# Optimization experiments

Measured on AMD Instinct MI355X. Metric: run time of the kernel, lower is better.

## Reference

```python
import jax, jax.numpy as jnp
import numpy as np

N = 100000
IN_PLANES = 64
OUT_PLANES = 64
SHARE = 8
NSAMPLE = 16


def setup_inputs() -> dict:
    key = jax.random.key(0)
    ks = jax.random.split(key, 20)
    f32 = jnp.float32
    s = lambda fan_in: 1.0 / np.sqrt(fan_in)
    inp = {}
    inp['p'] = jax.random.normal(ks[0], (N, 3), f32)
    inp['x'] = jax.random.normal(ks[1], (N, IN_PLANES), f32)
    inp['knn_idx'] = jax.random.randint(ks[2], (N, NSAMPLE), 0, N, jnp.int64)
    # channelMixMLPs01: Linear(3+in, nsample) -> ReLU -> Bilinear(ns, ns, ns)
    inp['W01'] = jax.random.uniform(ks[3], (3 + IN_PLANES, NSAMPLE), f32, -s(3 + IN_PLANES), s(3 + IN_PLANES))
    inp['b01'] = jnp.zeros((NSAMPLE,), f32)
    inp['Wbil'] = jax.random.uniform(ks[4], (NSAMPLE, NSAMPLE, NSAMPLE), f32, -s(NSAMPLE), s(NSAMPLE))
    inp['bbil'] = jnp.zeros((NSAMPLE,), f32)
    # linear_p: Linear(3,3) -> BN(3) -> ReLU -> Linear(3, out)
    inp['Wp1'] = jax.random.uniform(ks[5], (3, 3), f32, -s(3), s(3))
    inp['bp1'] = jnp.zeros((3,), f32)
    inp['bnp_s'] = jnp.ones((3,), f32)   # BN folded (inference): scale = gamma/sqrt(var+eps)
    inp['bnp_b'] = jnp.zeros((3,), f32)  # shift = beta - mean*scale
    inp['Wp2'] = jax.random.uniform(ks[6], (3, OUT_PLANES), f32, -s(3), s(3))
    inp['bp2'] = jnp.zeros((OUT_PLANES,), f32)
    # channelMixMLPs02
    mid = OUT_PLANES
    inp['W2a'] = jax.random.uniform(ks[7], (2 * NSAMPLE, mid), f32, -s(2 * NSAMPLE), s(2 * NSAMPLE))
    inp['bn2a_s'] = jnp.ones((mid,), f32)
    inp['bn2a_b'] = jnp.zeros((mid,), f32)
    inp['W2b'] = jax.random.uniform(ks[8], (mid, mid // SHARE), f32, -s(mid), s(mid))
    inp['bn2b_s'] = jnp.ones((mid // SHARE,), f32)
    inp['bn2b_b'] = jnp.zeros((mid // SHARE,), f32)
    inp['W2c'] = jax.random.uniform(ks[9], (mid // SHARE, OUT_PLANES // SHARE), f32, -s(mid // SHARE), s(mid // SHARE))
    inp['b2c'] = jnp.zeros((OUT_PLANES // SHARE,), f32)
    # channelMixMLPs03: Linear(in, out)
    inp['W3'] = jax.random.uniform(ks[10], (IN_PLANES, OUT_PLANES), f32, -s(IN_PLANES), s(IN_PLANES))
    inp['b3'] = jnp.zeros((OUT_PLANES,), f32)
    return inp


def reference(p, x, knn_idx, W01, b01, Wbil, bbil, Wp1, bp1, bnp_s, bnp_b,
              Wp2, bp2, W2a, bn2a_s, bn2a_b, W2b, bn2b_s, bn2b_b, W2c, b2c,
              W3, b3):
    n, k = knn_idx.shape
    out_planes = W3.shape[1]
    share = SHARE
    # queryandgroup(use_xyz=True): gather neighbors, relative xyz concat features
    p_r = p[knn_idx] - p[:, None, :]                      # [n,k,3]
    x_knn_in = jnp.concatenate([p_r, x[knn_idx]], -1)     # [n,k,3+in]
    xf = x_knn_in.reshape(n * k, -1)
    # channelMixMLPs01: Linear -> ReLU -> Bilinear(e, e)
    e = jax.nn.relu(xf @ W01 + b01)                       # [nk, ns]
    e = jnp.einsum('ni,oij,nj->no', e, Wbil, e) + bbil    # [nk, ns]
    # linear_p on relative coords
    pe = p_r.reshape(-1, 3) @ Wp1 + bp1
    pe = jax.nn.relu(pe * bnp_s + bnp_b)
    pe = pe @ Wp2 + bp2                                   # [nk, out]
    p_embed = pe.reshape(n, k, out_planes)
    # shrink_p: (n k (a b)) -> sum over a -> (nk, b=nsample)
    a = out_planes // k
    shrink = pe.reshape(n * k, a, k).sum(1)               # [nk, ns]
    ef = jnp.concatenate([e, shrink], -1)                 # [nk, 2*ns]
    # channelMixMLPs02
    h = jax.nn.relu((ef @ W2a) * bn2a_s + bn2a_b)
    h = jax.nn.relu((h @ W2b) * bn2b_s + bn2b_b)
    h = h @ W2c + b2c                                     # [nk, out/share]
    w = jax.nn.softmax(h.reshape(n, k, -1), axis=1)       # softmax over neighbors
    # channelMixMLPs03 then gather
    x_v = (x @ W3 + b3)[knn_idx]                          # [n,k,out]
    x_knn = (x_v + p_embed).reshape(n, k, share, out_planes // share)
    x_knn = (x_knn * w[:, :, None, :]).reshape(n, k, out_planes)
    x_out = x_knn.sum(1)                                  # [n,out]
    return (x_out, x_knn, knn_idx, p_r)
```

## Files before the change

### kernel.cpp

```cpp
#include <hip/hip_runtime.h>

#define NPTS 100000
#define NK   1600000

typedef __attribute__((ext_vector_type(8))) short bf16x8;
typedef __attribute__((ext_vector_type(4))) float f32x4;
typedef union { bf16x8 v; unsigned u[4]; } fragu;

#define MFMA(a,b,c) __builtin_amdgcn_mfma_f32_16x16x32_bf16((a),(b),(c),0,0,0)

#define WS_W01  0
#define WS_WBIL 1536
#define WS_W2A  5632
#define WS_W2B  7680
#define WS_WPE  8704
#define WS_BYTES 21504

__device__ inline unsigned cvtpk(float lo, float hi) {
  unsigned r;
  asm("v_cvt_pk_bf16_f32 %0, %1, %2" : "=v"(r) : "v"(lo), "v"(hi));
  return r;
}
__device__ inline short bfr(float f) {
  unsigned u = __float_as_uint(f);
  u += 0x7fff + ((u >> 16) & 1);
  return (short)(u >> 16);
}
__device__ inline float bflo(unsigned u) { return __uint_as_float(u << 16); }
__device__ inline float bfhi(unsigned u) { return __uint_as_float(u & 0xffff0000u); }

__global__ __launch_bounds__(256) void k_prep(
    const float* __restrict__ W01, const float* __restrict__ b01,
    const float* __restrict__ Wbil,
    const float* __restrict__ W2a, const float* __restrict__ W2b,
    const float* __restrict__ Wp2, const float* __restrict__ bp2,
    short* __restrict__ ws)
{
  const int t = threadIdx.x;
  for (int i = t; i < 3 * 512; i += 256) {
    int tt = i & 7, l = (i >> 3) & 63, kc = i >> 9;
    int o = l & 15, k = kc * 32 + ((l >> 4) << 3) + tt;
    float v = 0.f;
    if (k < 64) v = W01[(3 + k) * 16 + o];
    else if (k < 67) v = W01[(k - 64) * 16 + o];
    else if (k == 67) v = b01[o];
    ws[WS_W01 + i] = bfr(v);
  }
  for (int i = t; i < 8 * 512; i += 256) {
    int tt = i & 7, l = (i >> 3) & 63, kc = i >> 9;
    int o = l & 15, k = kc * 32 + ((l >> 4) << 3) + tt;
    ws[WS_WBIL + i] = bfr(Wbil[o * 256 + k]);
  }
  for (int i = t; i < 4 * 512; i += 256) {
    int tt = i & 7, l = (i >> 3) & 63, nt = i >> 9;
    int c = nt * 16 + (l & 15), k = ((l >> 4) << 3) + tt;
    ws[WS_W2A + i] = bfr(W2a[k * 64 + c]);
  }
  for (int i = t; i < 2 * 512; i += 256) {
    int tt = i & 7, l = (i >> 3) & 63, kc = i >> 9;
    int m = l & 15, k = kc * 32 + ((l >> 4) << 3) + tt;
    ws[WS_W2B + i] = bfr(m < 8 ? W2b[k * 8 + m] : 0.f);
  }
  for (int i = t; i < 4 * 512; i += 256) {
    int tt = i & 7, l = (i >> 3) & 63, nt = i >> 9;
    int c = nt * 16 + (l & 15), k = ((l >> 4) << 3) + tt;
    float v = 0.f;
    if (k < 3) v = Wp2[k * 64 + c]; else if (k == 3) v = bp2[c];
    ws[WS_WPE + i] = bfr(v);
  }
}

__global__ __launch_bounds__(256) void k_xw3(
    const float* __restrict__ x, const float* __restrict__ W3,
    const float* __restrict__ b3, float* __restrict__ y)
{
  int t = blockIdx.x * 256 + threadIdx.x;
  int i = __builtin_amdgcn_readfirstlane(t >> 6);
  int c = t & 63;
  if (i >= NPTS) return;
  const float* xr = x + i * 64;
  float acc = b3[c];
#pragma unroll
  for (int k = 0; k < 64; ++k)
    acc = fmaf(xr[k], W3[k * 64 + c], acc);
  y[i * 64 + c] = acc;
}

__global__ __launch_bounds__(256, 5) void k_main(
    const float* __restrict__ p, const float* __restrict__ x,
    const int* __restrict__ knn, const short* __restrict__ wsf,
    const float* __restrict__ Wp1, const float* __restrict__ bp1,
    const float* __restrict__ bnp_s, const float* __restrict__ bnp_b,
    const float* __restrict__ bbil,
    const float* __restrict__ bn2a_s, const float* __restrict__ bn2a_b,
    const float* __restrict__ bn2b_s, const float* __restrict__ bn2b_b,
    const float* __restrict__ W2c, const float* __restrict__ b2c,
    const float* __restrict__ Wp2, const float* __restrict__ bp2,
    const float* __restrict__ y,
    float* __restrict__ x_out, float* __restrict__ x_knn,
    float* __restrict__ knn_f, float* __restrict__ p_r)
{
  const int tid  = threadIdx.x;
  const int lane = tid & 63;
  const int mloc = lane & 15;
  const int kblk = lane >> 4;
  const int row  = blockIdx.x * 256 + tid;
  const int n    = row >> 4;
  const int j    = row & 15;
  const int idx  = knn[row];

  const float pr0 = p[idx * 3 + 0] - p[n * 3 + 0];
  const float pr1 = p[idx * 3 + 1] - p[n * 3 + 1];
  const float pr2 = p[idx * 3 + 2] - p[n * 3 + 2];

  float q0, q1, q2;
  {
    float v0 = bp1[0] + pr0 * Wp1[0] + pr1 * Wp1[3] + pr2 * Wp1[6];
    float v1 = bp1[1] + pr0 * Wp1[1] + pr1 * Wp1[4] + pr2 * Wp1[7];
    float v2 = bp1[2] + pr0 * Wp1[2] + pr1 * Wp1[5] + pr2 * Wp1[8];
    q0 = fmaxf(fmaf(v0, bnp_s[0], bnp_b[0]), 0.f);
    q1 = fmaxf(fmaf(v1, bnp_s[1], bnp_b[1]), 0.f);
    q2 = fmaxf(fmaf(v2, bnp_s[2], bnp_b[2]), 0.f);
  }

#define FR(off, idx_) (((const bf16x8*)wsf)[(off) / 8 + (idx_)])

  unsigned epk[4][2];
  {
    bf16x8 bw0 = FR(WS_W01, 0 * 64 + lane);
    bf16x8 bw1 = FR(WS_W01, 1 * 64 + lane);
    bf16x8 bw2 = FR(WS_W01, 2 * 64 + lane);
    const float4* x4 = (const float4*)x;
#pragma unroll
    for (int g = 0; g < 4; ++g) {
      const int src = g * 16 + mloc;
      int   ridx = __shfl(idx, src, 64);
      float p0s  = __shfl(pr0, src, 64);
      float p1s  = __shfl(pr1, src, 64);
      float p2s  = __shfl(pr2, src, 64);
      f32x4 acc = {0.f, 0.f, 0.f, 0.f};
      {
        float4 xa = x4[ridx * 16 + kblk * 2];
        float4 xb = x4[ridx * 16 + kblk * 2 + 1];
        fragu B;
        B.u[0] = cvtpk(xa.x, xa.y); B.u[1] = cvtpk(xa.z, xa.w);
        B.u[2] = cvtpk(xb.x, xb.y); B.u[3] = cvtpk(xb.z, xb.w);
        acc = MFMA(bw0, B.v, acc);
      }
      {
        float4 xa = x4[ridx * 16 + 8 + kblk * 2];
        float4 xb = x4[ridx * 16 + 9 + kblk * 2];
        fragu B;
        B.u[0] = cvtpk(xa.x, xa.y); B.u[1] = cvtpk(xa.z, xa.w);
        B.u[2] = cvtpk(xb.x, xb.y); B.u[3] = cvtpk(xb.z, xb.w);
        acc = MFMA(bw1, B.v, acc);
      }
      {
        fragu B;
        B.u[0] = (kblk == 0) ? cvtpk(p0s, p1s) : 0u;
        B.u[1] = (kblk == 0) ? cvtpk(p2s, 1.f) : 0u;
        B.u[2] = 0u; B.u[3] = 0u;
        acc = MFMA(bw2, B.v, acc);
      }
      epk[g][0] = cvtpk(fmaxf(acc[0], 0.f), fmaxf(acc[1], 0.f));
      epk[g][1] = cvtpk(fmaxf(acc[2], 0.f), fmaxf(acc[3], 0.f));
    }
  }

  unsigned h2p[4][2];
#pragma unroll
  for (int g = 0; g < 4; ++g) {
    float er[16];
    {
      unsigned a0 = __shfl(epk[g][0], mloc, 64);
      unsigned a1 = __shfl(epk[g][1], mloc, 64);
      unsigned b0 = __shfl(epk[g][0], mloc + 16, 64);
      unsigned b1 = __shfl(epk[g][1], mloc + 16, 64);
      unsigned c0 = __shfl(epk[g][0], mloc + 32, 64);
      unsigned c1 = __shfl(epk[g][1], mloc + 32, 64);
      unsigned d0 = __shfl(epk[g][0], mloc + 48, 64);
      unsigned d1 = __shfl(epk[g][1], mloc + 48, 64);
      er[0] = bflo(a0);  er[1] = bfhi(a0);  er[2]  = bflo(a1); er[3]  = bfhi(a1);
      er[4] = bflo(b0);  er[5] = bfhi(b0);  er[6]  = bflo(b1); er[7]  = bfhi(b1);
      er[8] = bflo(c0);  er[9] = bfhi(c0);  er[10] = bflo(c1); er[11] = bfhi(c1);
      er[12] = bflo(d0); er[13] = bfhi(d0); er[14] = bflo(d1); er[15] = bfhi(d1);
    }
    const int jhsel = kblk & 1, ihsel = kblk >> 1;
    float ej[8];
#pragma unroll
    for (int t = 0; t < 8; ++t) ej[t] = jhsel ? er[8 + t] : er[t];
    f32x4 acc2;
    {
      f32x4 bb = *(const f32x4*)&bbil[kblk * 4];
      acc2 = bb;
#pragma unroll
      for (int kc = 0; kc < 8; ++kc) {
        bf16x8 wb = FR(WS_WBIL, kc * 64 + lane);
        float ei = ihsel ? er[2 * kc + 1] : er[2 * kc];
        fragu B;
        B.u[0] = cvtpk(ei * ej[0], ei * ej[1]);
        B.u[1] = cvtpk(ei * ej[2], ei * ej[3]);
        B.u[2] = cvtpk(ei * ej[4], ei * ej[5]);
        B.u[3] = cvtpk(ei * ej[6], ei * ej[7]);
        acc2 = MFMA(wb, B.v, acc2);
      }
    }
    f32x4 shq;
    {
      const int src = g * 16 + mloc;
      float q0s = __shfl(q0, src, 64);
      float q1s = __shfl(q1, src, 64);
      float q2s = __shfl(q2, src, 64);
      fragu B;
      B.u[0] = (kblk == 0) ? cvtpk(q0s, q1s) : 0u;
      B.u[1] = (kblk == 0) ? cvtpk(q2s, 1.f) : 0u;
      B.u[2] = 0u; B.u[3] = 0u;
      f32x4 z = {0.f, 0.f, 0.f, 0.f};
      f32x4 s0 = MFMA(FR(WS_WPE, 0 * 64 + lane), B.v, z);
      f32x4 s1 = MFMA(FR(WS_WPE, 1 * 64 + lane), B.v, z);
      f32x4 s2 = MFMA(FR(WS_WPE, 2 * 64 + lane), B.v, z);
      f32x4 s3 = MFMA(FR(WS_WPE, 3 * 64 + lane), B.v, z);
#pragma unroll
      for (int r = 0; r < 4; ++r) shq[r] = s0[r] + s1[r] + s2[r] + s3[r];
    }
    unsigned pe2_0 = cvtpk(acc2[0], acc2[1]);
    unsigned pe2_1 = cvtpk(acc2[2], acc2[3]);
    unsigned psh_0 = cvtpk(shq[0], shq[1]);
    unsigned psh_1 = cvtpk(shq[2], shq[3]);
    fragu Bef;
    {
      const int s1l = mloc + 32 * (kblk & 1);
      const int s2l = s1l + 16;
      unsigned a0 = __shfl(pe2_0, s1l, 64);
      unsigned a1 = __shfl(pe2_1, s1l, 64);
      unsigned a2 = __shfl(pe2_0, s2l, 64);
      unsigned a3 = __shfl(pe2_1, s2l, 64);
      unsigned b0 = __shfl(psh_0, s1l, 64);
      unsigned b1 = __shfl(psh_1, s1l, 64);
      unsigned b2 = __shfl(psh_0, s2l, 64);
      unsigned b3 = __shfl(psh_1, s2l, 64);
      const bool lo2 = (kblk < 2);
      Bef.u[0] = lo2 ? a0 : b0; Bef.u[1] = lo2 ? a1 : b1;
      Bef.u[2] = lo2 ? a2 : b2; Bef.u[3] = lo2 ? a3 : b3;
    }
    unsigned pha[8];
#pragma unroll
    for (int nt = 0; nt < 4; ++nt) {
      bf16x8 wa = FR(WS_W2A, nt * 64 + lane);
      f32x4 z = {0.f, 0.f, 0.f, 0.f};
      f32x4 c = MFMA(wa, Bef.v, z);
      f32x4 sA = *(const f32x4*)&bn2a_s[nt * 16 + kblk * 4];
      f32x4 bA = *(const f32x4*)&bn2a_b[nt * 16 + kblk * 4];
      float h0 = fmaxf(fmaf(c[0], sA[0], bA[0]), 0.f);
      float h1 = fmaxf(fmaf(c[1], sA[1], bA[1]), 0.f);
      float h2 = fmaxf(fmaf(c[2], sA[2], bA[2]), 0.f);
      float h3 = fmaxf(fmaf(c[3], sA[3], bA[3]), 0.f);
      pha[nt * 2 + 0] = cvtpk(h0, h1);
      pha[nt * 2 + 1] = cvtpk(h2, h3);
    }
    {
      const int sAl = mloc + 32 * (kblk & 1);
      const int sBl = sAl + 16;
      const bool lo2 = (kblk < 2);
      fragu B0, B1;
      {
        unsigned a0 = __shfl(pha[0], sAl, 64), a1 = __shfl(pha[1], sAl, 64);
        unsigned a2 = __shfl(pha[0], sBl, 64), a3 = __shfl(pha[1], sBl, 64);
        unsigned b0 = __shfl(pha[2], sAl, 64), b1 = __shfl(pha[3], sAl, 64);
        unsigned b2 = __shfl(pha[2], sBl, 64), b3 = __shfl(pha[3], sBl, 64);
        B0.u[0] = lo2 ? a0 : b0; B0.u[1] = lo2 ? a1 : b1;
        B0.u[2] = lo2 ? a2 : b2; B0.u[3] = lo2 ? a3 : b3;
      }
      {
        unsigned a0 = __shfl(pha[4], sAl, 64), a1 = __shfl(pha[5], sAl, 64);
        unsigned a2 = __shfl(pha[4], sBl, 64), a3 = __shfl(pha[5], sBl, 64);
        unsigned b0 = __shfl(pha[6], sAl, 64), b1 = __shfl(pha[7], sAl, 64);
        unsigned b2 = __shfl(pha[6], sBl, 64), b3 = __shfl(pha[7], sBl, 64);
        B1.u[0] = lo2 ? a0 : b0; B1.u[1] = lo2 ? a1 : b1;
        B1.u[2] = lo2 ? a2 : b2; B1.u[3] = lo2 ? a3 : b3;
      }
      f32x4 acc3 = {0.f, 0.f, 0.f, 0.f};
      acc3 = MFMA(FR(WS_W2B, 0 * 64 + lane), B0.v, acc3);
      acc3 = MFMA(FR(WS_W2B, 1 * 64 + lane), B1.v, acc3);
      f32x4 s = *(const f32x4*)&bn2b_s[(kblk & 1) * 4];
      f32x4 b = *(const f32x4*)&bn2b_b[(kblk & 1) * 4];
      float v0 = fmaxf(fmaf(acc3[0], s[0], b[0]), 0.f);
      float v1 = fmaxf(fmaf(acc3[1], s[1], b[1]), 0.f);
      float v2 = fmaxf(fmaf(acc3[2], s[2], b[2]), 0.f);
      float v3 = fmaxf(fmaf(acc3[3], s[3], b[3]), 0.f);
      h2p[g][0] = cvtpk(v0, v1);
      h2p[g][1] = cvtpk(v2, v3);
    }
  }

  unsigned hp0 = 0, hp1 = 0, hp2 = 0, hp3 = 0;
#pragma unroll
  for (int g = 0; g < 4; ++g) {
    unsigned t0 = __shfl(h2p[g][0], mloc, 64);
    unsigned t1 = __shfl(h2p[g][1], mloc, 64);
    unsigned t2 = __shfl(h2p[g][0], mloc + 16, 64);
    unsigned t3 = __shfl(h2p[g][1], mloc + 16, 64);
    const bool mine = (kblk == g);
    hp0 = mine ? t0 : hp0; hp1 = mine ? t1 : hp1;
    hp2 = mine ? t2 : hp2; hp3 = mine ? t3 : hp3;
  }
  float h2r[8];
  h2r[0] = bflo(hp0); h2r[1] = bfhi(hp0); h2r[2] = bflo(hp1); h2r[3] = bfhi(hp1);
  h2r[4] = bflo(hp2); h2r[5] = bfhi(hp2); h2r[6] = bflo(hp3); h2r[7] = bfhi(hp3);

  float h3[8];
#pragma unroll
  for (int b = 0; b < 8; ++b) h3[b] = b2c[b];
#pragma unroll
  for (int m = 0; m < 8; ++m) {
    float r = h2r[m];
#pragma unroll
    for (int b = 0; b < 8; ++b) h3[b] = fmaf(r, W2c[m * 8 + b], h3[b]);
  }
  float wv[8];
#pragma unroll
  for (int b = 0; b < 8; ++b) {
    float mx = h3[b];
    mx = fmaxf(mx, __shfl_xor(mx, 1, 16));
    mx = fmaxf(mx, __shfl_xor(mx, 2, 16));
    mx = fmaxf(mx, __shfl_xor(mx, 4, 16));
    mx = fmaxf(mx, __shfl_xor(mx, 8, 16));
    float ex = __expf(h3[b] - mx);
    float s = ex;
    s += __shfl_xor(s, 1, 16);
    s += __shfl_xor(s, 2, 16);
    s += __shfl_xor(s, 4, 16);
    s += __shfl_xor(s, 8, 16);
    wv[b] = ex / s;
  }

  const float4* y4 = (const float4*)y;
  float* xkrow = x_knn + (long long)row * 64;
  float xo[4] = {0.f, 0.f, 0.f, 0.f};
#pragma unroll
  for (int h = 0; h < 2; ++h) {
    float4 yv[8];
#pragma unroll
    for (int u = 0; u < 8; ++u) yv[u] = y4[idx * 16 + h * 8 + u];
    f32x4 vout[8];
#pragma unroll
    for (int u = 0; u < 8; ++u) {
      float comp[4] = {yv[u].x, yv[u].y, yv[u].z, yv[u].w};
#pragma unroll
      for (int cc = 0; cc < 4; ++cc) {
        const int c = h * 32 + u * 4 + cc;
        float pe = bp2[c] + q0 * Wp2[c] + q1 * Wp2[64 + c] + q2 * Wp2[128 + c];
        float val = (comp[cc] + pe) * wv[c & 7];
        vout[u][cc] = val;
        float r = val;
        r += __shfl_xor(r, 1, 16);
        r += __shfl_xor(r, 2, 16);
        r += __shfl_xor(r, 4, 16);
        r += __shfl_xor(r, 8, 16);
        if (j == (c & 15)) xo[c >> 4] = r;
      }
    }
#pragma unroll
    for (int u = 0; u < 8; ++u)
      *(f32x4*)(xkrow + h * 32 + u * 4) = vout[u];
  }
#pragma unroll
  for (int g = 0; g < 4; ++g)
    x_out[n * 64 + g * 16 + j] = xo[g];

  if (knn_f) {
    knn_f[row] = (float)idx;
    p_r[row * 3 + 0] = pr0;
    p_r[row * 3 + 1] = pr1;
    p_r[row * 3 + 2] = pr2;
  }
}

__global__ __launch_bounds__(256) void k_tail(
    const float* __restrict__ p, const int* __restrict__ knn,
    float* __restrict__ knn_f, float* __restrict__ p_r)
{
  int row = blockIdx.x * 256 + threadIdx.x;
  if (row >= NK) return;
  int n = row >> 4;
  int idx = knn[row];
  knn_f[row] = (float)idx;
  p_r[row * 3 + 0] = p[idx * 3 + 0] - p[n * 3 + 0];
  p_r[row * 3 + 1] = p[idx * 3 + 1] - p[n * 3 + 1];
  p_r[row * 3 + 2] = p[idx * 3 + 2] - p[n * 3 + 2];
}

extern "C" void kernel_launch(void* const* d_in, const int* in_sizes, int n_in,
                              void* d_out, int out_size, void* d_ws, size_t ws_size,
                              hipStream_t stream)
{
  const float* p    = (const float*)d_in[0];
  const float* x    = (const float*)d_in[1];
  const int*   knn  = (const int*)d_in[2];
  const float* W01  = (const float*)d_in[3];
  const float* b01  = (const float*)d_in[4];
  const float* Wbil = (const float*)d_in[5];
  const float* bbil = (const float*)d_in[6];
  const float* Wp1  = (const float*)d_in[7];
  const float* bp1  = (const float*)d_in[8];
  const float* bnps = (const float*)d_in[9];
  const float* bnpb = (const float*)d_in[10];
  const float* Wp2  = (const float*)d_in[11];
  const float* bp2  = (const float*)d_in[12];
  const float* W2a  = (const float*)d_in[13];
  const float* s2a  = (const float*)d_in[14];
  const float* b2a  = (const float*)d_in[15];
  const float* W2b  = (const float*)d_in[16];
  const float* s2b  = (const float*)d_in[17];
  const float* b2b  = (const float*)d_in[18];
  const float* W2c  = (const float*)d_in[19];
  const float* b2c  = (const float*)d_in[20];
  const float* W3   = (const float*)d_in[21];
  const float* b3   = (const float*)d_in[22];

  float* outF  = (float*)d_out;
  float* x_out = outF;
  float* x_knn = outF + 6400000;
  float* knn_f = outF + 108800000;
  float* p_r   = outF + 110400000;
  short* wsf   = (short*)d_ws;

  const size_t yBytes = (size_t)NPTS * 64 * sizeof(float);
  const bool bigWs = ws_size >= (size_t)WS_BYTES + yBytes;
  float* y = bigWs ? (float*)((char*)d_ws + WS_BYTES) : knn_f;

  k_prep<<<1, 256, 0, stream>>>(W01, b01, Wbil, W2a, W2b, Wp2, bp2, wsf);
  k_xw3<<<25000, 256, 0, stream>>>(x, W3, b3, y);
  k_main<<<6250, 256, 0, stream>>>(p, x, knn, wsf, Wp1, bp1, bnps, bnpb,
                                   bbil, s2a, b2a, s2b, b2b, W2c, b2c,
                                   Wp2, bp2, y, x_out, x_knn,
                                   bigWs ? knn_f : (float*)nullptr,
                                   bigWs ? p_r : (float*)nullptr);
  if (!bigWs)
    k_tail<<<6250, 256, 0, stream>>>(p, knn, knn_f, p_r);
}
```

Measured before the change: 417.2 us.

## Replace shfl with bpermute/DPP and use butterfly transpose-reduce for x_out

Replaces generic __shfl calls with direct ds_bpermute intrinsics, which drops the index arithmetic __shfl adds. Softmax max/sum reductions now use DPP row-ror ops and a hardware reciprocal. The 64-channel cross-neighbor sum now uses a recursive-halving butterfly (DPP quad permutes plus ds_swizzle) in place of 64 independent 4-step xor reductions, cutting cross-lane ops from about 256 to about 31 per half. It adds select logic and some register pressure, and rcp is less exact than a true divide.

```diff
diff --git a/kernel.cpp b/kernel.cpp
--- a/kernel.cpp
+++ b/kernel.cpp
@@ -28,6 +28,26 @@
 }
 __device__ inline float bflo(unsigned u) { return __uint_as_float(u << 16); }
 __device__ inline float bfhi(unsigned u) { return __uint_as_float(u & 0xffff0000u); }
+
+template<int CTRL>
+__device__ inline float fdpp(float x) {
+  return __int_as_float(__builtin_amdgcn_update_dpp(
+      0, __float_as_int(x), CTRL, 0xF, 0xF, true));
+}
+template<int XM>
+__device__ inline float fswz(float x) {
+  return __int_as_float(__builtin_amdgcn_ds_swizzle(
+      __float_as_int(x), 0x1F | (XM << 10)));
+}
+__device__ inline unsigned bpermu(int src, unsigned v) {
+  return (unsigned)__builtin_amdgcn_ds_bpermute(src << 2, (int)v);
+}
+__device__ inline float bpermf(int src, float v) {
+  return __int_as_float(__builtin_amdgcn_ds_bpermute(src << 2, __float_as_int(v)));
+}
+__device__ inline int bpermi(int src, int v) {
+  return __builtin_amdgcn_ds_bpermute(src << 2, v);
+}
 
 __global__ __launch_bounds__(256) void k_prep(
     const float* __restrict__ W01, const float* __restrict__ b01,
@@ -134,10 +154,10 @@
 #pragma unroll
     for (int g = 0; g < 4; ++g) {
       const int src = g * 16 + mloc;
-      int   ridx = __shfl(idx, src, 64);
-      float p0s  = __shfl(pr0, src, 64);
-      float p1s  = __shfl(pr1, src, 64);
-      float p2s  = __shfl(pr2, src, 64);
+      int   ridx = bpermi(src, idx);
+      float p0s  = bpermf(src, pr0);
+      float p1s  = bpermf(src, pr1);
+      float p2s  = bpermf(src, pr2);
       f32x4 acc = {0.f, 0.f, 0.f, 0.f};
       {
         float4 xa = x4[ridx * 16 + kblk * 2];
@@ -172,14 +192,14 @@
   for (int g = 0; g < 4; ++g) {
     float er[16];
     {
-      unsigned a0 = __shfl(epk[g][0], mloc, 64);
-      unsigned a1 = __shfl(epk[g][1], mloc, 64);
-      unsigned b0 = __shfl(epk[g][0], mloc + 16, 64);
-      unsigned b1 = __shfl(epk[g][1], mloc + 16, 64);
-      unsigned c0 = __shfl(epk[g][0], mloc + 32, 64);
-      unsigned c1 = __shfl(epk[g][1], mloc + 32, 64);
-      unsigned d0 = __shfl(epk[g][0], mloc + 48, 64);
-      unsigned d1 = __shfl(epk[g][1], mloc + 48, 64);
+      unsigned a0 = bpermu(mloc,      epk[g][0]);
+      unsigned a1 = bpermu(mloc,      epk[g][1]);
+      unsigned b0 = bpermu(mloc + 16, epk[g][0]);
+      unsigned b1 = bpermu(mloc + 16, epk[g][1]);
+      unsigned c0 = bpermu(mloc + 32, epk[g][0]);
+      unsigned c1 = bpermu(mloc + 32, epk[g][1]);
+      unsigned d0 = bpermu(mloc + 48, epk[g][0]);
+      unsigned d1 = bpermu(mloc + 48, epk[g][1]);
       er[0] = bflo(a0);  er[1] = bfhi(a0);  er[2]  = bflo(a1); er[3]  = bfhi(a1);
       er[4] = bflo(b0);  er[5] = bfhi(b0);  er[6]  = bflo(b1); er[7]  = bfhi(b1);
       er[8] = bflo(c0);  er[9] = bfhi(c0);  er[10] = bflo(c1); er[11] = bfhi(c1);
@@ -208,9 +228,9 @@
     f32x4 shq;
     {
       const int src = g * 16 + mloc;
-      float q0s = __shfl(q0, src, 64);
-      float q1s = __shfl(q1, src, 64);
-      float q2s = __shfl(q2, src, 64);
+      float q0s = bpermf(src, q0);
+      float q1s = bpermf(src, q1);
+      float q2s = bpermf(src, q2);
       fragu B;
       B.u[0] = (kblk == 0) ? cvtpk(q0s, q1s) : 0u;
       B.u[1] = (kblk == 0) ? cvtpk(q2s, 1.f) : 0u;
@@ -231,14 +251,14 @@
     {
       const int s1l = mloc + 32 * (kblk & 1);
       const int s2l = s1l + 16;
-      unsigned a0 = __shfl(pe2_0, s1l, 64);
-      unsigned a1 = __shfl(pe2_1, s1l, 64);
-      unsigned a2 = __shfl(pe2_0, s2l, 64);
-      unsigned a3 = __shfl(pe2_1, s2l, 64);
-      unsigned b0 = __shfl(psh_0, s1l, 64);
-      unsigned b1 = __shfl(psh_1, s1l, 64);
-      unsigned b2 = __shfl(psh_0, s2l, 64);
-      unsigned b3 = __shfl(psh_1, s2l, 64);
+      unsigned a0 = bpermu(s1l, pe2_0);
+      unsigned a1 = bpermu(s1l, pe2_1);
+      unsigned a2 = bpermu(s2l, pe2_0);
+      unsigned a3 = bpermu(s2l, pe2_1);
+      unsigned b0 = bpermu(s1l, psh_0);
+      unsigned b1 = bpermu(s1l, psh_1);
+      unsigned b2 = bpermu(s2l, psh_0);
+      unsigned b3 = bpermu(s2l, psh_1);
       const bool lo2 = (kblk < 2);
       Bef.u[0] = lo2 ? a0 : b0; Bef.u[1] = lo2 ? a1 : b1;
       Bef.u[2] = lo2 ? a2 : b2; Bef.u[3] = lo2 ? a3 : b3;
@@ -264,18 +284,18 @@
       const bool lo2 = (kblk < 2);
       fragu B0, B1;
       {
-        unsigned a0 = __shfl(pha[0], sAl, 64), a1 = __shfl(pha[1], sAl, 64);
-        unsigned a2 = __shfl(pha[0], sBl, 64), a3 = __shfl(pha[1], sBl, 64);
-        unsigned b0 = __shfl(pha[2], sAl, 64), b1 = __shfl(pha[3], sAl, 64);
-        unsigned b2 = __shfl(pha[2], sBl, 64), b3 = __shfl(pha[3], sBl, 64);
+        unsigned a0 = bpermu(sAl, pha[0]), a1 = bpermu(sAl, pha[1]);
+        unsigned a2 = bpermu(sBl, pha[0]), a3 = bpermu(sBl, pha[1]);
+        unsigned b0 = bpermu(sAl, pha[2]), b1 = bpermu(sAl, pha[3]);
+        unsigned b2 = bpermu(sBl, pha[2]), b3 = bpermu(sBl, pha[3]);
         B0.u[0] = lo2 ? a0 : b0; B0.u[1] = lo2 ? a1 : b1;
         B0.u[2] = lo2 ? a2 : b2; B0.u[3] = lo2 ? a3 : b3;
       }
       {
-        unsigned a0 = __shfl(pha[4], sAl, 64), a1 = __shfl(pha[5], sAl, 64);
-        unsigned a2 = __shfl(pha[4], sBl, 64), a3 = __shfl(pha[5], sBl, 64);
-        unsigned b0 = __shfl(pha[6], sAl, 64), b1 = __shfl(pha[7], sAl, 64);
-        unsigned b2 = __shfl(pha[6], sBl, 64), b3 = __shfl(pha[7], sBl, 64);
+        unsigned a0 = bpermu(sAl, pha[4]), a1 = bpermu(sAl, pha[5]);
+        unsigned a2 = bpermu(sBl, pha[4]), a3 = bpermu(sBl, pha[5]);
+        unsigned b0 = bpermu(sAl, pha[6]), b1 = bpermu(sAl, pha[7]);
+        unsigned b2 = bpermu(sBl, pha[6]), b3 = bpermu(sBl, pha[7]);
         B1.u[0] = lo2 ? a0 : b0; B1.u[1] = lo2 ? a1 : b1;
         B1.u[2] = lo2 ? a2 : b2; B1.u[3] = lo2 ? a3 : b3;
       }
@@ -296,10 +316,10 @@
   unsigned hp0 = 0, hp1 = 0, hp2 = 0, hp3 = 0;
 #pragma unroll
   for (int g = 0; g < 4; ++g) {
-    unsigned t0 = __shfl(h2p[g][0], mloc, 64);
-    unsigned t1 = __shfl(h2p[g][1], mloc, 64);
-    unsigned t2 = __shfl(h2p[g][0], mloc + 16, 64);
-    unsigned t3 = __shfl(h2p[g][1], mloc + 16, 64);
+    unsigned t0 = bpermu(mloc,      h2p[g][0]);
+    unsigned t1 = bpermu(mloc,      h2p[g][1]);
+    unsigned t2 = bpermu(mloc + 16, h2p[g][0]);
+    unsigned t3 = bpermu(mloc + 16, h2p[g][1]);
     const bool mine = (kblk == g);
     hp0 = mine ? t0 : hp0; hp1 = mine ? t1 : hp1;
     hp2 = mine ? t2 : hp2; hp3 = mine ? t3 : hp3;
@@ -321,48 +341,72 @@
 #pragma unroll
   for (int b = 0; b < 8; ++b) {
     float mx = h3[b];
-    mx = fmaxf(mx, __shfl_xor(mx, 1, 16));
-    mx = fmaxf(mx, __shfl_xor(mx, 2, 16));
-    mx = fmaxf(mx, __shfl_xor(mx, 4, 16));
-    mx = fmaxf(mx, __shfl_xor(mx, 8, 16));
+    mx = fmaxf(mx, fdpp<0x128>(mx));
+    mx = fmaxf(mx, fdpp<0x124>(mx));
+    mx = fmaxf(mx, fdpp<0x122>(mx));
+    mx = fmaxf(mx, fdpp<0x121>(mx));
     float ex = __expf(h3[b] - mx);
     float s = ex;
-    s += __shfl_xor(s, 1, 16);
-    s += __shfl_xor(s, 2, 16);
-    s += __shfl_xor(s, 4, 16);
-    s += __shfl_xor(s, 8, 16);
-    wv[b] = ex / s;
+    s = s + fdpp<0x128>(s);
+    s = s + fdpp<0x124>(s);
+    s = s + fdpp<0x122>(s);
+    s = s + fdpp<0x121>(s);
+    wv[b] = ex * __builtin_amdgcn_rcpf(s);
   }
 
   const float4* y4 = (const float4*)y;
   float* xkrow = x_knn + (long long)row * 64;
-  float xo[4] = {0.f, 0.f, 0.f, 0.f};
+  float xo[4];
 #pragma unroll
   for (int h = 0; h < 2; ++h) {
     float4 yv[8];
 #pragma unroll
     for (int u = 0; u < 8; ++u) yv[u] = y4[idx * 16 + h * 8 + u];
-    f32x4 vout[8];
+    float v[32];
 #pragma unroll
     for (int u = 0; u < 8; ++u) {
       float comp[4] = {yv[u].x, yv[u].y, yv[u].z, yv[u].w};
+      f32x4 st;
 #pragma unroll
       for (int cc = 0; cc < 4; ++cc) {
         const int c = h * 32 + u * 4 + cc;
         float pe = bp2[c] + q0 * Wp2[c] + q1 * Wp2[64 + c] + q2 * Wp2[128 + c];
         float val = (comp[cc] + pe) * wv[c & 7];
-        vout[u][cc] = val;
-        float r = val;
-        r += __shfl_xor(r, 1, 16);
-        r += __shfl_xor(r, 2, 16);
-        r += __shfl_xor(r, 4, 16);
-        r += __shfl_xor(r, 8, 16);
-        if (j == (c & 15)) xo[c >> 4] = r;
-      }
-    }
-#pragma unroll
-    for (int u = 0; u < 8; ++u)
-      *(f32x4*)(xkrow + h * 32 + u * 4) = vout[u];
+        v[u * 4 + cc] = val;
+        st[cc] = val;
+      }
+      *(f32x4*)(xkrow + h * 32 + u * 4) = st;
+    }
+    const bool b0 = (j & 1), b1 = (j & 2), b2 = (j & 4), b3 = (j & 8);
+    float v1[16];
+#pragma unroll
+    for (int q = 0; q < 16; ++q) {
+      float snd = b0 ? v[2 * q] : v[2 * q + 1];
+      float rcv = fdpp<0xB1>(snd);
+      v1[q] = (b0 ? v[2 * q + 1] : v[2 * q]) + rcv;
+    }
+    float v2[8];
+#pragma unroll
+    for (int r = 0; r < 8; ++r) {
+      float snd = b1 ? v1[2 * r] : v1[2 * r + 1];
+      float rcv = fdpp<0x4E>(snd);
+      v2[r] = (b1 ? v1[2 * r + 1] : v1[2 * r]) + rcv;
+    }
+    float v3[4];
+#pragma unroll
+    for (int s = 0; s < 4; ++s) {
+      float snd = b2 ? v2[2 * s] : v2[2 * s + 1];
+      float rcv = fswz<4>(snd);
+      v3[s] = (b2 ? v2[2 * s + 1] : v2[2 * s]) + rcv;
+    }
+    {
+      float s0 = b3 ? v3[0] : v3[1];
+      float s1 = b3 ? v3[2] : v3[3];
+      float r0 = fswz<8>(s0);
+      float r1 = fswz<8>(s1);
+      xo[2 * h]     = (b3 ? v3[1] : v3[0]) + r0;
+      xo[2 * h + 1] = (b3 ? v3[3] : v3[2]) + r1;
+    }
   }
 #pragma unroll
   for (int g = 0; g < 4; ++g)
```

Measured after the change: 402.3 us. 1.04x faster.
